# Performance work log

Measured on AMD Instinct MI355X. Metric: run time of the kernel, lower is better.

## Reference

```python
import jax, jax.numpy as jnp
import numpy as np

N, F, E = 100000, 128, 1600000


def setup_inputs() -> dict:
    key = jax.random.key(0)
    ks = jax.random.split(key, 10)
    s = 1.0 / np.sqrt(F)
    return {
        "x": jax.random.normal(ks[0], (N, F), jnp.float32),
        "edge_index": jax.random.randint(ks[1], (2, E), 0, N),
        "edge_weight": jax.random.uniform(ks[2], (E,), jnp.float32),
        # EvolveGCNO initial weight (1, F, F) -> squeezed to (F, F)
        "initial_weight": jax.random.normal(ks[3], (F, F), jnp.float32) * s,
        # torch.nn.GRU(F, F) params, gate order (r, z, n)
        "gru_w_ih": jax.random.uniform(ks[4], (3 * F, F), jnp.float32, -s, s),
        "gru_w_hh": jax.random.uniform(ks[5], (3 * F, F), jnp.float32, -s, s),
        "gru_b_ih": jax.random.uniform(ks[6], (3 * F,), jnp.float32, -s, s),
        "gru_b_hh": jax.random.uniform(ks[7], (3 * F,), jnp.float32, -s, s),
        # Linear(F, 1)
        "lin_w": jax.random.uniform(ks[8], (1, F), jnp.float32, -s, s),
        "lin_b": jax.random.uniform(ks[9], (1,), jnp.float32, -s, s),
    }


def _evolve_weight(W0, w_ih, w_hh, b_ih, b_hh):
    # One GRU step: input = W0 rows (batch=F), hidden = W0 rows (first call of EvolveGCNO)
    gi = W0 @ w_ih.T + b_ih  # (F, 3F)
    gh = W0 @ w_hh.T + b_hh
    i_r, i_z, i_n = jnp.split(gi, 3, axis=-1)
    h_r, h_z, h_n = jnp.split(gh, 3, axis=-1)
    r = jax.nn.sigmoid(i_r + h_r)
    z = jax.nn.sigmoid(i_z + h_z)
    n = jnp.tanh(i_n + r * h_n)
    return (1.0 - z) * n + z * W0  # (F, F)


def reference(x, edge_index, edge_weight, initial_weight, gru_w_ih, gru_w_hh,
              gru_b_ih, gru_b_hh, lin_w, lin_b):
    W = _evolve_weight(initial_weight, gru_w_ih, gru_w_hh, gru_b_ih, gru_b_hh)
    n_nodes = x.shape[0]
    row, col = edge_index[0], edge_index[1]  # source, target
    # gcn_norm: add self loops (weight 1), sym-normalize D^-1/2 (A+I) D^-1/2
    loop = jnp.arange(n_nodes)
    row = jnp.concatenate([row, loop])
    col = jnp.concatenate([col, loop])
    w = jnp.concatenate([edge_weight, jnp.ones((n_nodes,), x.dtype)])
    deg = jax.ops.segment_sum(w, col, num_segments=n_nodes)
    dinv = jnp.where(deg > 0, jax.lax.rsqrt(deg), 0.0)
    norm = dinv[row] * w * dinv[col]  # (E+N,)
    xw = x @ W  # (N, F)
    # gather at sources, weighted scatter-add at targets
    h = jax.ops.segment_sum(norm[:, None] * xw[row], col, num_segments=n_nodes)
    h = jax.nn.relu(h)
    return (h @ lin_w.T + lin_b)[:, 0]  # (N,)
```

## Files before the change

### kernel.cpp

```cpp
#include <hip/hip_runtime.h>

#define F 128
#define DEG_SCALE 16777216.0f
#define DEG_INV   (1.0f / 16777216.0f)
#define BUCK_BITS 7
#define BUCK_COLS 128
#define CAP 2304
#define EPT 8
#define WB_STRIDE 136

typedef _Float16 half8 __attribute__((ext_vector_type(8)));
typedef float f32x4 __attribute__((ext_vector_type(4)));

__global__ __launch_bounds__(256) void init_kernel(
    int* __restrict__ cursor, int NZ, int NBUK,
    const float* __restrict__ W0, const float* __restrict__ wih,
    const float* __restrict__ whh, const float* __restrict__ bih,
    const float* __restrict__ bhh, float* __restrict__ W) {
  __shared__ float w0row[2][F];
  int b = blockIdx.x;
  if (b < NZ) {
    int i = b * 256 + threadIdx.x;
    if (i < NBUK) cursor[i] = 0;
    return;
  }
  int half = threadIdx.x >> 7;
  int j = threadIdx.x & 127;
  int i = (b - NZ) * 2 + half;
  w0row[half][j] = W0[i * F + j];
  __syncthreads();
  float ar = 0, az = 0, an = 0, br = 0, bz = 0, bn = 0;
  const float* wi_r = wih + (size_t)j * F;
  const float* wi_z = wih + (size_t)(j + F) * F;
  const float* wi_n = wih + (size_t)(j + 2 * F) * F;
  const float* wh_r = whh + (size_t)j * F;
  const float* wh_z = whh + (size_t)(j + F) * F;
  const float* wh_n = whh + (size_t)(j + 2 * F) * F;
#pragma unroll 4
  for (int k = 0; k < F; ++k) {
    float a = w0row[half][k];
    ar = fmaf(a, wi_r[k], ar);
    az = fmaf(a, wi_z[k], az);
    an = fmaf(a, wi_n[k], an);
    br = fmaf(a, wh_r[k], br);
    bz = fmaf(a, wh_z[k], bz);
    bn = fmaf(a, wh_n[k], bn);
  }
  float gr = ar + bih[j] + br + bhh[j];
  float gz = az + bih[j + F] + bz + bhh[j + F];
  float r = 1.f / (1.f + expf(-gr));
  float z = 1.f / (1.f + expf(-gz));
  float n = tanhf(an + bih[j + 2 * F] + r * (bn + bhh[j + 2 * F]));
  W[i * F + j] = (1.f - z) * n + z * w0row[half][j];
}

__global__ __launch_bounds__(1024) void gemm_bin(
    const float* __restrict__ x, const float* __restrict__ W,
    _Float16* __restrict__ xwh, int N, int GB,
    const int* __restrict__ row, const int* __restrict__ col,
    const float* __restrict__ ew, int* __restrict__ cursor,
    uint2* __restrict__ binned, int E, int NBUK) {
  __shared__ _Float16 Wb[F * WB_STRIDE];
  __shared__ int cnt[1024];
  __shared__ int base[1024];
  int t = threadIdx.x;

  if ((int)blockIdx.x >= GB) {
    cnt[t] = 0;
    __syncthreads();
    int e0 = ((int)blockIdx.x - GB) * (1024 * EPT) + t;
    int cc[EPT];
    int lrank[EPT];
#pragma unroll
    for (int k = 0; k < EPT; ++k) {
      int e = e0 + k * 1024;
      if (e < E) {
        cc[k] = col[e];
        lrank[k] = atomicAdd(&cnt[cc[k] >> BUCK_BITS], 1);
      } else cc[k] = -1;
    }
    __syncthreads();
    if (t < NBUK) {
      int c = cnt[t];
      base[t] = c ? atomicAdd(&cursor[t], c) : 0;
    }
    __syncthreads();
#pragma unroll
    for (int k = 0; k < EPT; ++k) {
      if (cc[k] >= 0) {
        int e = e0 + k * 1024;
        int b = cc[k] >> BUCK_BITS;
        int pos = base[b] + lrank[k];
        if (pos < CAP) {
          unsigned cl = (unsigned)(cc[k] & (BUCK_COLS - 1));
          binned[(size_t)b * CAP + pos] =
              make_uint2((unsigned)row[e] | (cl << 17), __float_as_uint(ew[e]));
        }
      }
    }
    return;
  }

  for (int idx = t; idx < F * F; idx += 1024) {
    int k = idx >> 7, n = idx & 127;
    Wb[n * WB_STRIDE + k] = (_Float16)W[idx];
  }
  __syncthreads();

  int lane = t & 63, wave = t >> 6;
  int ln = lane & 15, q = lane >> 4;
  int rowb = blockIdx.x * 256 + wave * 16;
  int i = rowb + ln;
  int iclamp = (i < N) ? i : N - 1;
  const float* xp = x + (size_t)iclamp * F + q * 8;

  half8 a[4];
#pragma unroll
  for (int tt = 0; tt < 4; ++tt) {
    float4 v0 = *(const float4*)(xp + 32 * tt);
    float4 v1 = *(const float4*)(xp + 32 * tt + 4);
    half8 av;
    av[0] = (_Float16)v0.x; av[1] = (_Float16)v0.y;
    av[2] = (_Float16)v0.z; av[3] = (_Float16)v0.w;
    av[4] = (_Float16)v1.x; av[5] = (_Float16)v1.y;
    av[6] = (_Float16)v1.z; av[7] = (_Float16)v1.w;
    a[tt] = av;
  }

  f32x4 acc[8];
#pragma unroll
  for (int nt = 0; nt < 8; ++nt) acc[nt] = (f32x4){0.f, 0.f, 0.f, 0.f};

#pragma unroll
  for (int nt = 0; nt < 8; ++nt) {
#pragma unroll
    for (int tt = 0; tt < 4; ++tt) {
      half8 bfrag = *(const half8*)&Wb[(nt * 16 + ln) * WB_STRIDE + tt * 32 + q * 8];
      acc[nt] = __builtin_amdgcn_mfma_f32_16x16x32_f16(a[tt], bfrag, acc[nt], 0, 0, 0);
    }
  }

#pragma unroll
  for (int nt = 0; nt < 8; ++nt) {
#pragma unroll
    for (int r = 0; r < 4; ++r) {
      int rowi = rowb + q * 4 + r;
      if (rowi < N) xwh[(size_t)rowi * F + nt * 16 + ln] = (_Float16)acc[nt][r];
    }
  }
}

__global__ __launch_bounds__(256) void csr_deg(
    const uint2* __restrict__ binned, const int* __restrict__ cursor,
    float* __restrict__ dinv, int* __restrict__ cnts, int N) {
  __shared__ unsigned long long acc[BUCK_COLS];
  int b = blockIdx.x;
  int tid = threadIdx.x;
  if (tid < BUCK_COLS) acc[tid] = 0ull;
  __syncthreads();
  int cnt = cursor[b];
  if (cnt > CAP) cnt = CAP;
  const uint2* src = binned + (size_t)b * CAP;
  for (int i = tid; i < cnt; i += 256) {
    uint2 rec = src[i];
    int cl = rec.x >> 17;
    unsigned fx = (unsigned)(__uint_as_float(rec.y) * DEG_SCALE);
    atomicAdd(&acc[cl], ((unsigned long long)1 << 32) | (unsigned long long)fx);
  }
  __syncthreads();
  if (tid < BUCK_COLS) {
    int node = b * BUCK_COLS + tid;
    if (node < N) {
      unsigned long long pk = acc[tid];
      float deg = (float)(unsigned)(pk & 0xffffffffull) * DEG_INV;
      dinv[node] = rsqrtf(deg + 1.0f);
      cnts[node] = (int)(pk >> 32);
    }
  }
}

__global__ __launch_bounds__(256) void csr_fill(
    const uint2* __restrict__ binned, const int* __restrict__ cursor,
    const int* __restrict__ cnts, const float* __restrict__ dinv,
    int* __restrict__ offs, uint2* __restrict__ pairs, int N, int NBUK) {
  __shared__ float dinvL[BUCK_COLS];
  __shared__ int sc[BUCK_COLS];
  __shared__ int woff[BUCK_COLS];
  __shared__ int wsum[4];
  __shared__ uint2 sorted[CAP + BUCK_COLS];
  int b = blockIdx.x;
  int tid = threadIdx.x;
  int partial = 0;
  for (int i = tid; i < b; i += 256) partial += min(cursor[i], CAP);
#pragma unroll
  for (int m = 32; m; m >>= 1) partial += __shfl_xor(partial, m);
  if ((tid & 63) == 0) wsum[tid >> 6] = partial;
  __syncthreads();
  int bstart = b * BUCK_COLS + wsum[0] + wsum[1] + wsum[2] + wsum[3];

  int node0 = b * BUCK_COLS;
  int cvt1 = 0;
  if (tid < BUCK_COLS) {
    int node = node0 + tid;
    if (node < N) {
      cvt1 = cnts[node] + 1;
      dinvL[tid] = dinv[node];
    }
    sc[tid] = cvt1;
  }
  __syncthreads();
  for (int off = 1; off < BUCK_COLS; off <<= 1) {
    int x = 0;
    if (tid < BUCK_COLS && tid >= off) x = sc[tid - off];
    __syncthreads();
    if (tid < BUCK_COLS) sc[tid] += x;
    __syncthreads();
  }
  if (tid < BUCK_COLS) {
    int node = node0 + tid;
    if (node < N) {
      int rel0 = sc[tid] - cvt1;
      offs[node] = bstart + rel0;
      float dv = dinvL[tid];
      sorted[rel0] = make_uint2((unsigned)node << 8, __float_as_uint(dv * dv));
      woff[tid] = rel0 + 1;
    }
  }
  __syncthreads();
  int cnt = cursor[b];
  if (cnt > CAP) cnt = CAP;
  const uint2* src = binned + (size_t)b * CAP;
  for (int i = tid; i < cnt; i += 256) {
    uint2 rec = src[i];
    int cl = rec.x >> 17;
    unsigned r = rec.x & 0x1ffffu;
    float wp = __uint_as_float(rec.y) * dinvL[cl] * dinv[r];
    int pos = atomicAdd(&woff[cl], 1);
    sorted[pos] = make_uint2(r << 8, __float_as_uint(wp));
  }
  __syncthreads();
  int tot = sc[BUCK_COLS - 1];
  for (int i = tid; i < tot; i += 256) pairs[bstart + i] = sorted[i];
  if (b == NBUK - 1) {
    if (tid == 0) offs[N] = bstart + tot;
    if (tid < 16) pairs[bstart + tot + tid] = make_uint2(0u, 0u);
  }
}

__global__ __launch_bounds__(256) void gather_out(
    const uint2* __restrict__ pairs, const int* __restrict__ offs,
    const char* __restrict__ xwb, const float* __restrict__ linw,
    const float* __restrict__ linb, float* __restrict__ out, int N) {
  int wave = threadIdx.x >> 6;
  int lane = threadIdx.x & 63;
  int node = blockIdx.x * 4 + wave;
  if (node >= N) return;
  int c = lane & 15;
  int q = lane >> 4;

  const char* xb = xwb + (c << 4);
  half8 acca = {0, 0, 0, 0, 0, 0, 0, 0};
  half8 accb = {0, 0, 0, 0, 0, 0, 0, 0};

  int start = offs[node], end = offs[node + 1];
  for (int it = start + q; it < end; it += 16) {
    uint2 p0 = pairs[it];
    uint2 p1 = pairs[it + 4];
    uint2 p2 = pairs[it + 8];
    uint2 p3 = pairs[it + 12];
    half8 x0 = *(const half8*)(xb + p0.x);
    half8 x1 = *(const half8*)(xb + p1.x);
    half8 x2 = *(const half8*)(xb + p2.x);
    half8 x3 = *(const half8*)(xb + p3.x);
    float f0 = __uint_as_float(p0.y);
    float f1 = (it + 4 < end) ? __uint_as_float(p1.y) : 0.f;
    float f2 = (it + 8 < end) ? __uint_as_float(p2.y) : 0.f;
    float f3 = (it + 12 < end) ? __uint_as_float(p3.y) : 0.f;
    _Float16 h0 = (_Float16)f0, h1 = (_Float16)f1;
    _Float16 h2 = (_Float16)f2, h3 = (_Float16)f3;
    half8 n0 = {h0, h0, h0, h0, h0, h0, h0, h0};
    half8 n1 = {h1, h1, h1, h1, h1, h1, h1, h1};
    half8 n2 = {h2, h2, h2, h2, h2, h2, h2, h2};
    half8 n3 = {h3, h3, h3, h3, h3, h3, h3, h3};
    acca += x0 * n0;
    accb += x1 * n1;
    acca += x2 * n2;
    accb += x3 * n3;
  }

  float acc[8];
#pragma unroll
  for (int j = 0; j < 8; ++j) acc[j] = (float)acca[j] + (float)accb[j];

#pragma unroll
  for (int j = 0; j < 8; ++j) {
    acc[j] += __shfl_xor(acc[j], 16);
    acc[j] += __shfl_xor(acc[j], 32);
  }

  const float4* lw4 = (const float4*)linw;
  float4 la = lw4[c * 2];
  float4 lb = lw4[c * 2 + 1];
  float p = fmaxf(acc[0], 0.f) * la.x + fmaxf(acc[1], 0.f) * la.y +
            fmaxf(acc[2], 0.f) * la.z + fmaxf(acc[3], 0.f) * la.w +
            fmaxf(acc[4], 0.f) * lb.x + fmaxf(acc[5], 0.f) * lb.y +
            fmaxf(acc[6], 0.f) * lb.z + fmaxf(acc[7], 0.f) * lb.w;
#pragma unroll
  for (int m = 8; m; m >>= 1) p += __shfl_xor(p, m);

  if (lane == 0) out[node] = p + linb[0];
}

extern "C" void kernel_launch(void* const* d_in, const int* in_sizes, int n_in,
                              void* d_out, int out_size, void* d_ws, size_t ws_size,
                              hipStream_t stream) {
  const float* x    = (const float*)d_in[0];
  const int*   ei   = (const int*)d_in[1];
  const float* ew   = (const float*)d_in[2];
  const float* W0   = (const float*)d_in[3];
  const float* wih  = (const float*)d_in[4];
  const float* whh  = (const float*)d_in[5];
  const float* bih  = (const float*)d_in[6];
  const float* bhh  = (const float*)d_in[7];
  const float* linw = (const float*)d_in[8];
  const float* linb = (const float*)d_in[9];

  int N = in_sizes[0] / F;
  int E = in_sizes[2];
  const int* row = ei;
  const int* col = ei + E;
  int NBUK = (N + BUCK_COLS - 1) / BUCK_COLS;
  int total = E + N;

  char* p = (char*)d_ws;
  auto alloc = [&](size_t bytes) {
    char* q = p;
    p += (bytes + 255) & ~(size_t)255;
    return q;
  };
  float*    W      = (float*)alloc((size_t)F * F * 4);
  int*      cursor = (int*)alloc((size_t)NBUK * 4);
  float*    dinv   = (float*)alloc((size_t)N * 4);
  int*      cnts   = (int*)alloc((size_t)N * 4);
  int*      offs   = (int*)alloc(((size_t)N + 1) * 4);
  uint2*    binned = (uint2*)alloc((size_t)NBUK * CAP * 8);
  uint2*    pairs  = (uint2*)alloc(((size_t)total + 16) * 8);
  _Float16* xwh    = (_Float16*)alloc((size_t)N * F * 2);

  int NZ = (NBUK + 255) / 256;
  init_kernel<<<NZ + 64, 256, 0, stream>>>(cursor, NZ, NBUK, W0, wih, whh, bih, bhh, W);

  int GB = (N + 255) / 256;
  int BB = (E + 1024 * EPT - 1) / (1024 * EPT);
  gemm_bin<<<GB + BB, 1024, 0, stream>>>(x, W, xwh, N, GB,
                                         row, col, ew, cursor, binned, E, NBUK);

  csr_deg<<<NBUK, 256, 0, stream>>>(binned, cursor, dinv, cnts, N);
  csr_fill<<<NBUK, 256, 0, stream>>>(binned, cursor, cnts, dinv, offs, pairs, N, NBUK);

  gather_out<<<(N + 3) / 4, 256, 0, stream>>>(pairs, offs, (const char*)xwh,
                                              linw, linb, (float*)d_out, N);
}
```

Baseline: 258.4 us.

## Fuse CSR fill and gather into one per-bucket kernel using shared-memory edge lists

Merges csr_fill and gather_out into a single kernel. Each block sorts its bucket's edges by target in shared memory and then aggregates the neighbour features straight from that sorted list, so the global pairs/offs arrays and the cross-bucket prefix scan go away. Accumulation now runs in fp32 instead of packed fp16, and the self-loop is folded in as an initial term. The cost is far fewer blocks (about 782) with one 16-lane group handling 4 nodes each, which lowers parallelism and memory-level parallelism for the random gathers.

Measured after the change: 257.9 us. No clear change (-0.2%).

```diff
diff --git a/kernel.cpp b/kernel.cpp
--- a/kernel.cpp
+++ b/kernel.cpp
@@ -179,34 +179,27 @@
   }
 }
 
-__global__ __launch_bounds__(256) void csr_fill(
+__global__ __launch_bounds__(512) void csr_gather(
     const uint2* __restrict__ binned, const int* __restrict__ cursor,
     const int* __restrict__ cnts, const float* __restrict__ dinv,
-    int* __restrict__ offs, uint2* __restrict__ pairs, int N, int NBUK) {
+    const char* __restrict__ xwb, const float* __restrict__ linw,
+    const float* __restrict__ linb, float* __restrict__ out, int N) {
   __shared__ float dinvL[BUCK_COLS];
   __shared__ int sc[BUCK_COLS];
   __shared__ int woff[BUCK_COLS];
-  __shared__ int wsum[4];
-  __shared__ uint2 sorted[CAP + BUCK_COLS];
+  __shared__ uint2 sorted[CAP + 4];
   int b = blockIdx.x;
   int tid = threadIdx.x;
-  int partial = 0;
-  for (int i = tid; i < b; i += 256) partial += min(cursor[i], CAP);
-#pragma unroll
-  for (int m = 32; m; m >>= 1) partial += __shfl_xor(partial, m);
-  if ((tid & 63) == 0) wsum[tid >> 6] = partial;
-  __syncthreads();
-  int bstart = b * BUCK_COLS + wsum[0] + wsum[1] + wsum[2] + wsum[3];
-
   int node0 = b * BUCK_COLS;
-  int cvt1 = 0;
+
+  int cvt = 0;
   if (tid < BUCK_COLS) {
     int node = node0 + tid;
     if (node < N) {
-      cvt1 = cnts[node] + 1;
+      cvt = cnts[node];
       dinvL[tid] = dinv[node];
-    }
-    sc[tid] = cvt1;
+    } else dinvL[tid] = 0.f;
+    sc[tid] = cvt;
   }
   __syncthreads();
   for (int off = 1; off < BUCK_COLS; off <<= 1) {
@@ -216,21 +209,13 @@
     if (tid < BUCK_COLS) sc[tid] += x;
     __syncthreads();
   }
-  if (tid < BUCK_COLS) {
-    int node = node0 + tid;
-    if (node < N) {
-      int rel0 = sc[tid] - cvt1;
-      offs[node] = bstart + rel0;
-      float dv = dinvL[tid];
-      sorted[rel0] = make_uint2((unsigned)node << 8, __float_as_uint(dv * dv));
-      woff[tid] = rel0 + 1;
-    }
-  }
-  __syncthreads();
+  if (tid < BUCK_COLS) woff[tid] = sc[tid] - cvt;
+  __syncthreads();
+
   int cnt = cursor[b];
   if (cnt > CAP) cnt = CAP;
   const uint2* src = binned + (size_t)b * CAP;
-  for (int i = tid; i < cnt; i += 256) {
+  for (int i = tid; i < cnt; i += 512) {
     uint2 rec = src[i];
     int cl = rec.x >> 17;
     unsigned r = rec.x & 0x1ffffu;
@@ -240,75 +225,61 @@
   }
   __syncthreads();
   int tot = sc[BUCK_COLS - 1];
-  for (int i = tid; i < tot; i += 256) pairs[bstart + i] = sorted[i];
-  if (b == NBUK - 1) {
-    if (tid == 0) offs[N] = bstart + tot;
-    if (tid < 16) pairs[bstart + tot + tid] = make_uint2(0u, 0u);
-  }
-}
-
-__global__ __launch_bounds__(256) void gather_out(
-    const uint2* __restrict__ pairs, const int* __restrict__ offs,
-    const char* __restrict__ xwb, const float* __restrict__ linw,
-    const float* __restrict__ linb, float* __restrict__ out, int N) {
-  int wave = threadIdx.x >> 6;
-  int lane = threadIdx.x & 63;
-  int node = blockIdx.x * 4 + wave;
-  if (node >= N) return;
-  int c = lane & 15;
-  int q = lane >> 4;
-
-  const char* xb = xwb + (c << 4);
-  half8 acca = {0, 0, 0, 0, 0, 0, 0, 0};
-  half8 accb = {0, 0, 0, 0, 0, 0, 0, 0};
-
-  int start = offs[node], end = offs[node + 1];
-  for (int it = start + q; it < end; it += 16) {
-    uint2 p0 = pairs[it];
-    uint2 p1 = pairs[it + 4];
-    uint2 p2 = pairs[it + 8];
-    uint2 p3 = pairs[it + 12];
-    half8 x0 = *(const half8*)(xb + p0.x);
-    half8 x1 = *(const half8*)(xb + p1.x);
-    half8 x2 = *(const half8*)(xb + p2.x);
-    half8 x3 = *(const half8*)(xb + p3.x);
-    float f0 = __uint_as_float(p0.y);
-    float f1 = (it + 4 < end) ? __uint_as_float(p1.y) : 0.f;
-    float f2 = (it + 8 < end) ? __uint_as_float(p2.y) : 0.f;
-    float f3 = (it + 12 < end) ? __uint_as_float(p3.y) : 0.f;
-    _Float16 h0 = (_Float16)f0, h1 = (_Float16)f1;
-    _Float16 h2 = (_Float16)f2, h3 = (_Float16)f3;
-    half8 n0 = {h0, h0, h0, h0, h0, h0, h0, h0};
-    half8 n1 = {h1, h1, h1, h1, h1, h1, h1, h1};
-    half8 n2 = {h2, h2, h2, h2, h2, h2, h2, h2};
-    half8 n3 = {h3, h3, h3, h3, h3, h3, h3, h3};
-    acca += x0 * n0;
-    accb += x1 * n1;
-    acca += x2 * n2;
-    accb += x3 * n3;
-  }
-
-  float acc[8];
-#pragma unroll
-  for (int j = 0; j < 8; ++j) acc[j] = (float)acca[j] + (float)accb[j];
-
-#pragma unroll
-  for (int j = 0; j < 8; ++j) {
-    acc[j] += __shfl_xor(acc[j], 16);
-    acc[j] += __shfl_xor(acc[j], 32);
-  }
-
+  if (tid < 4) sorted[tot + tid] = make_uint2(0u, 0u);
+  __syncthreads();
+
+  int qid = tid >> 4;
+  int lq = tid & 15;
+  const char* xb = xwb + (lq << 4);
   const float4* lw4 = (const float4*)linw;
-  float4 la = lw4[c * 2];
-  float4 lb = lw4[c * 2 + 1];
-  float p = fmaxf(acc[0], 0.f) * la.x + fmaxf(acc[1], 0.f) * la.y +
-            fmaxf(acc[2], 0.f) * la.z + fmaxf(acc[3], 0.f) * la.w +
-            fmaxf(acc[4], 0.f) * lb.x + fmaxf(acc[5], 0.f) * lb.y +
-            fmaxf(acc[6], 0.f) * lb.z + fmaxf(acc[7], 0.f) * lb.w;
-#pragma unroll
-  for (int m = 8; m; m >>= 1) p += __shfl_xor(p, m);
-
-  if (lane == 0) out[node] = p + linb[0];
+  float4 la = lw4[lq * 2];
+  float4 lb = lw4[lq * 2 + 1];
+  float lbias = linb[0];
+
+  for (int c4 = 0; c4 < 4; ++c4) {
+    int cl = qid * 4 + c4;
+    int node = node0 + cl;
+    if (node >= N) break;
+    int s0 = cl ? sc[cl - 1] : 0;
+    int s1 = sc[cl];
+    float dv = dinvL[cl];
+    half8 xs = *(const half8*)(xb + ((unsigned)node << 8));
+    float sw = dv * dv;
+    float acc[8];
+#pragma unroll
+    for (int j = 0; j < 8; ++j) acc[j] = sw * (float)xs[j];
+
+    for (int e = s0; e < s1; e += 4) {
+      uint2 p0 = sorted[e];
+      uint2 p1 = sorted[e + 1];
+      uint2 p2 = sorted[e + 2];
+      uint2 p3 = sorted[e + 3];
+      half8 x0 = *(const half8*)(xb + p0.x);
+      half8 x1 = *(const half8*)(xb + p1.x);
+      half8 x2 = *(const half8*)(xb + p2.x);
+      half8 x3 = *(const half8*)(xb + p3.x);
+      float n0 = __uint_as_float(p0.y);
+      float n1 = (e + 1 < s1) ? __uint_as_float(p1.y) : 0.f;
+      float n2 = (e + 2 < s1) ? __uint_as_float(p2.y) : 0.f;
+      float n3 = (e + 3 < s1) ? __uint_as_float(p3.y) : 0.f;
+#pragma unroll
+      for (int j = 0; j < 8; ++j) acc[j] = fmaf(n0, (float)x0[j], acc[j]);
+#pragma unroll
+      for (int j = 0; j < 8; ++j) acc[j] = fmaf(n1, (float)x1[j], acc[j]);
+#pragma unroll
+      for (int j = 0; j < 8; ++j) acc[j] = fmaf(n2, (float)x2[j], acc[j]);
+#pragma unroll
+      for (int j = 0; j < 8; ++j) acc[j] = fmaf(n3, (float)x3[j], acc[j]);
+    }
+
+    float p = fmaxf(acc[0], 0.f) * la.x + fmaxf(acc[1], 0.f) * la.y +
+              fmaxf(acc[2], 0.f) * la.z + fmaxf(acc[3], 0.f) * la.w +
+              fmaxf(acc[4], 0.f) * lb.x + fmaxf(acc[5], 0.f) * lb.y +
+              fmaxf(acc[6], 0.f) * lb.z + fmaxf(acc[7], 0.f) * lb.w;
+#pragma unroll
+    for (int m = 8; m; m >>= 1) p += __shfl_xor(p, m);
+    if (lq == 0) out[node] = p + lbias;
+  }
 }
 
 extern "C" void kernel_launch(void* const* d_in, const int* in_sizes, int n_in,
@@ -330,7 +301,6 @@
   const int* row = ei;
   const int* col = ei + E;
   int NBUK = (N + BUCK_COLS - 1) / BUCK_COLS;
-  int total = E + N;
 
   char* p = (char*)d_ws;
   auto alloc = [&](size_t bytes) {
@@ -342,9 +312,7 @@
   int*      cursor = (int*)alloc((size_t)NBUK * 4);
   float*    dinv   = (float*)alloc((size_t)N * 4);
   int*      cnts   = (int*)alloc((size_t)N * 4);
-  int*      offs   = (int*)alloc(((size_t)N + 1) * 4);
   uint2*    binned = (uint2*)alloc((size_t)NBUK * CAP * 8);
-  uint2*    pairs  = (uint2*)alloc(((size_t)total + 16) * 8);
   _Float16* xwh    = (_Float16*)alloc((size_t)N * F * 2);
 
   int NZ = (NBUK + 255) / 256;
@@ -356,8 +324,8 @@
                                          row, col, ew, cursor, binned, E, NBUK);
 
   csr_deg<<<NBUK, 256, 0, stream>>>(binned, cursor, dinv, cnts, N);
-  csr_fill<<<NBUK, 256, 0, stream>>>(binned, cursor, cnts, dinv, offs, pairs, N, NBUK);
-
-  gather_out<<<(N + 3) / 4, 256, 0, stream>>>(pairs, offs, (const char*)xwh,
-                                              linw, linb, (float*)d_out, N);
-}
+
+  csr_gather<<<NBUK, 512, 0, stream>>>(binned, cursor, cnts, dinv,
+                                       (const char*)xwh, linw, linb,
+                                       (float*)d_out, N);
+}
```
